# Performance work log

Hardware: AMD Instinct MI355X
Metric: run time of the kernel (lower is better)

## Reference

```python
import jax, jax.numpy as jnp
import numpy as np

SQRT2 = 1.4142135623730951
MH_C = 0.8673250705840776  # (2/sqrt(3)) * pi**(-1/4), mexican-hat normalizer


def _bn(x, eps=1e-5):
    # BatchNorm (training-mode batch stats, default affine gamma=1, beta=0)
    mu = jnp.mean(x, axis=0, keepdims=True)
    var = jnp.var(x, axis=0, keepdims=True)
    return (x - mu) / jnp.sqrt(var + eps)


def setup_inputs() -> dict:
    key = jax.random.key(0)
    ks = jax.random.split(key, 10)
    N, F, E, B, OUT = 1024, 1024, 32768, 16, 10
    H = F // 2  # 512 after Haar DWT
    x = jax.random.normal(ks[0], (N, F), dtype=jnp.float32)
    edge_index = jax.random.randint(ks[1], (2, E), 0, N, dtype=jnp.int32)
    batch = jnp.sort(jax.random.randint(ks[2], (N,), 0, B, dtype=jnp.int32))
    w_att = jax.random.normal(ks[3], (2,), dtype=jnp.float32)  # Linear(2,1,bias=False)
    wk_scale = jnp.ones((H, H), dtype=jnp.float32)
    wk_trans = jax.random.normal(ks[4], (H, H), dtype=jnp.float32) * 0.1
    wk_wav_w = jax.random.normal(ks[5], (H, H), dtype=jnp.float32) * 0.05
    wk_base_w = jax.random.normal(ks[6], (H, H), dtype=jnp.float32) * 0.05
    fc1_w = jax.random.normal(ks[7], (512, F + H), dtype=jnp.float32) * 0.02
    fc1_b = jnp.zeros((512,), dtype=jnp.float32)
    fc2_w = jax.random.normal(ks[8], (OUT, 512), dtype=jnp.float32) * 0.02
    fc2_b = jnp.zeros((OUT,), dtype=jnp.float32)
    return {"x": x, "w_att": w_att, "wk_scale": wk_scale, "wk_trans": wk_trans,
            "wk_wav_w": wk_wav_w, "wk_base_w": wk_base_w, "fc1_w": fc1_w,
            "fc1_b": fc1_b, "fc2_w": fc2_w, "fc2_b": fc2_b,
            "edge_index": edge_index, "batch": batch, "num_graphs": B}


def reference(x, w_att, wk_scale, wk_trans, wk_wav_w, wk_base_w,
              fc1_w, fc1_b, fc2_w, fc2_b, edge_index, batch, num_graphs):
    N = x.shape[0]
    # --- WaveletAttention: Haar ('db1') DWT over the feature dim ---
    xe, xo = x[:, 0::2], x[:, 1::2]
    low = (xe + xo) / SQRT2            # [N, 512]
    high = (xe - xo) / SQRT2           # [N, 512]
    scores = jax.nn.sigmoid(low * w_att[0] + high * w_att[1])
    h = scores * low + (1.0 - scores) * high
    # --- GINConv aggregation (eps=0): self + sum of neighbor features ---
    src, dst = edge_index[0], edge_index[1]
    agg = h + jax.ops.segment_sum(h[src], dst, num_segments=N)  # [N, 512]
    # --- WavKAN layer 512->512 (mexican hat) ---
    xs = (agg[:, None, :] - wk_trans) / wk_scale                # [N, 512, 512]
    xs2 = xs * xs
    mh = MH_C * (1.0 - xs2) * jnp.exp(-0.5 * xs2)
    wav = jnp.einsum('noi,oi->no', mh, wk_wav_w)                # [N, 512]
    base = jax.nn.silu(agg) @ wk_base_w.T
    conv_out = _bn(wav + base)   # WavKAN-internal BatchNorm1d
    conv_out = _bn(conv_out)     # bn1 (dropout p=0 -> identity)
    # --- skip concat + bn2 ---
    z = _bn(jnp.concatenate([x, conv_out], axis=1))             # [N, 1536]
    # --- global mean pool over graphs ---
    sums = jax.ops.segment_sum(z, batch, num_segments=num_graphs)
    cnts = jax.ops.segment_sum(jnp.ones((N,), z.dtype), batch, num_segments=num_graphs)
    pooled = sums / jnp.maximum(cnts, 1.0)[:, None]             # [B, 1536]
    # --- classifier head (eval-mode dropout = identity) ---
    h1 = jax.nn.relu(pooled @ fc1_w.T + fc1_b)
    return h1 @ fc2_w.T + fc2_b
```

## Files before the change

### kernel.cpp

```cpp
#include <hip/hip_runtime.h>
#include <math.h>

#define N_NODES 1024
#define F_DIM   1024
#define H_DIM   512
#define E_EDGES 32768
#define B_GRAPHS 16
#define OUT_DIM 10
#define FH_DIM  1536
#define EPS 1e-5f
#define MH_C_D 0.8673250705840776
#define C2_D   0.72134752044448170368
#define C2_F   ((float)C2_D)
#define CSC    0.84932180028801904272f
#define WC2F   ((float)(MH_C_D / C2_D))
#define INV_SQRT2 0.70710678118654752440f

typedef float v2f __attribute__((ext_vector_type(2)));
typedef unsigned int u32;
typedef const __attribute__((address_space(1))) u32 gu32;
typedef __attribute__((address_space(3))) u32 lu32;

#if __has_builtin(__builtin_amdgcn_exp2f)
#define EXP2NEG(x) __builtin_amdgcn_exp2f(-(x))
#else
#define EXP2NEG(x) __expf(-0.69314718055994530942f * (x))
#endif

#define PK_FMA_BB(d, a, p) \
    asm("v_pk_fma_f32 %0, %1, %2, %2 op_sel:[0,0,1] op_sel_hi:[1,0,1]" \
        : "=v"(d) : "v"(a), "v"(p))
#define PK_MUL2(d, a, b) \
    asm("v_pk_mul_f32 %0, %1, %2" : "=v"(d) : "v"(a), "v"(b))
#define PK_WZC(d, s, k) \
    asm("v_pk_mul_f32 %0, %1, %2 op_sel:[0,0] op_sel_hi:[0,1]" \
        : "=v"(d) : "v"(s), "v"(k))
#define PK_FMA_HI_ACC(acc, s, p) \
    asm("v_pk_fma_f32 %0, %1, %2, %0 op_sel:[0,1,0] op_sel_hi:[1,1,1]" \
        : "+v"(acc) : "v"(s), "v"(p))

__global__ __launch_bounds__(256) void k_setup(const float* __restrict__ x,
                                               const float* __restrict__ watt,
                                               float* __restrict__ h,
                                               const float* __restrict__ scale,
                                               const float* __restrict__ trans,
                                               const float* __restrict__ ww,
                                               const float* __restrict__ bw,
                                               float* __restrict__ pk,
                                               float* __restrict__ zbase) {
    const int bid = blockIdx.x;
    const int t = threadIdx.x;
    if (bid < 2048) {
        int idx = bid * 256 + t;
        float2 p = ((const float2*)x)[idx];
        float lo = (p.x + p.y) * INV_SQRT2;
        float hi = (p.x - p.y) * INV_SQRT2;
        float tt = lo * watt[0] + hi * watt[1];
        float sc = 1.0f / (1.0f + __expf(-tt));
        h[idx] = sc * lo + (1.0f - sc) * hi;
    } else if (bid < 3072) {
        int g = (bid - 2048) * 256 + t;
        float iv = 1.0f / scale[g];
        float4 p;
        p.x = iv * CSC;
        p.y = -(trans[g] * iv * CSC);
        p.z = -(ww[g] * WC2F);
        p.w = bw[g];
        ((float4*)pk)[g] = p;
    } else {
        zbase[(bid - 3072) * 256 + t] = 0.0f;
    }
}

__global__ __launch_bounds__(256) void k_hx(const int* __restrict__ dst,
                                            int* __restrict__ deg,
                                            const float* __restrict__ x,
                                            float* __restrict__ xsum,
                                            float* __restrict__ xsum2) {
    const int bid = blockIdx.x;
    const int t = threadIdx.x;
    if (bid < 128) {
        int e = bid * 256 + t;
        atomicAdd(&deg[dst[e]], 1);
    } else {
        const int n0 = (bid - 128) * 16;
        float s[4] = {}, s2[4] = {};
        for (int r = 0; r < 16; ++r) {
            #pragma unroll
            for (int ch = 0; ch < 4; ++ch) {
                float v = x[(n0 + r) * F_DIM + ch * 256 + t];
                s[ch] += v; s2[ch] += v * v;
            }
        }
        #pragma unroll
        for (int ch = 0; ch < 4; ++ch) {
            unsafeAtomicAdd(&xsum[ch * 256 + t], s[ch]);
            unsafeAtomicAdd(&xsum2[ch * 256 + t], s2[ch]);
        }
    }
}

__global__ __launch_bounds__(1024) void k_scan(const int* __restrict__ deg,
                                               int* __restrict__ start,
                                               int* __restrict__ cursor) {
    __shared__ int wsum[16];
    int t = threadIdx.x;
    int lane = t & 63, wid = t >> 6;
    int v = deg[t];
    int x = v;
    #pragma unroll
    for (int off = 1; off < 64; off <<= 1) {
        int y = __shfl_up(x, off, 64);
        if (lane >= off) x += y;
    }
    if (lane == 63) wsum[wid] = x;
    __syncthreads();
    if (t < 16) {
        int w = wsum[t];
        int xs = w;
        #pragma unroll
        for (int off = 1; off < 16; off <<= 1) {
            int y = __shfl_up(xs, off, 64);
            if (t >= off) xs += y;
        }
        wsum[t] = xs - w;
    }
    __syncthreads();
    int excl = wsum[wid] + x - v;
    start[t] = excl;
    cursor[t] = excl;
}

__global__ __launch_bounds__(256) void k_fill(const int* __restrict__ src,
                                              const int* __restrict__ dst,
                                              int* __restrict__ cursor,
                                              int* __restrict__ elist) {
    int e = blockIdx.x * 256 + threadIdx.x;
    int slot = atomicAdd(&cursor[dst[e]], 1);
    elist[slot] = src[e];
}

__global__ __launch_bounds__(256) void k_gather(const float* __restrict__ h,
                                                const int* __restrict__ start,
                                                const int* __restrict__ deg,
                                                const int* __restrict__ elist,
                                                float* __restrict__ agg) {
    int d = blockIdx.x;
    int t = threadIdx.x;
    int st = start[d], dg = deg[d];
    const float2* h2 = (const float2*)h;
    float2 a = h2[d * 256 + t];
    int k = 0;
    for (; k + 4 <= dg; k += 4) {
        int s0 = elist[st + k];
        int s1 = elist[st + k + 1];
        int s2 = elist[st + k + 2];
        int s3 = elist[st + k + 3];
        float2 v0 = h2[s0 * 256 + t];
        float2 v1 = h2[s1 * 256 + t];
        float2 v2 = h2[s2 * 256 + t];
        float2 v3 = h2[s3 * 256 + t];
        a.x += (v0.x + v1.x) + (v2.x + v3.x);
        a.y += (v0.y + v1.y) + (v2.y + v3.y);
    }
    for (; k < dg; ++k) {
        int s0 = elist[st + k];
        float2 v0 = h2[s0 * 256 + t];
        a.x += v0.x; a.y += v0.y;
    }
    ((float2*)agg)[d * 256 + t] = a;
}

__global__ __launch_bounds__(256) void k_transpose(const float* __restrict__ agg,
                                                   float* __restrict__ aggT,
                                                   float* __restrict__ siluT) {
    __shared__ float tile[64 * 65];
    const int t = threadIdx.x;
    const int n0 = blockIdx.x * 64;
    const int i0 = blockIdx.y * 64;
    #pragma unroll
    for (int v = 0; v < 4; ++v) {
        int flat = v * 256 + t;
        int r = flat >> 4, c4 = flat & 15;
        float4 a = *(const float4*)&agg[(n0 + r) * H_DIM + i0 + c4 * 4];
        tile[(c4 * 4 + 0) * 65 + r] = a.x;
        tile[(c4 * 4 + 1) * 65 + r] = a.y;
        tile[(c4 * 4 + 2) * 65 + r] = a.z;
        tile[(c4 * 4 + 3) * 65 + r] = a.w;
    }
    __syncthreads();
    #pragma unroll
    for (int v = 0; v < 4; ++v) {
        int flat = v * 256 + t;
        int il = flat >> 4, c4 = flat & 15;
        float4 a;
        a.x = tile[il * 65 + c4 * 4 + 0];
        a.y = tile[il * 65 + c4 * 4 + 1];
        a.z = tile[il * 65 + c4 * 4 + 2];
        a.w = tile[il * 65 + c4 * 4 + 3];
        int g = (i0 + il) * N_NODES + n0 + c4 * 4;
        *(float4*)&aggT[g] = a;
        float4 s;
        s.x = a.x / (1.0f + __expf(-a.x));
        s.y = a.y / (1.0f + __expf(-a.y));
        s.z = a.z / (1.0f + __expf(-a.z));
        s.w = a.w / (1.0f + __expf(-a.w));
        *(float4*)&siluT[g] = s;
    }
}

#define TN 64
#define TO 32
#define KI 16
#define TOP (TO + 1)
#define ZSPLIT 4
#define ZLEN (H_DIM / ZSPLIT)
#define NSTG (ZLEN / KI)
__global__ __launch_bounds__(256) void k_wavelet(const float* __restrict__ aggT,
                                                 const float* __restrict__ siluT,
                                                 const float* __restrict__ pk,
                                                 float* __restrict__ vbp) {
    __shared__ float sA[2][KI * TN];
    __shared__ float sS[2][KI * TN];
    __shared__ float4 sP4[2][KI * TOP];

    const int t  = threadIdx.x;
    const int n0 = blockIdx.x * TN;
    const int o0 = blockIdx.y * TO;
    const int z0 = blockIdx.z * ZLEN;
    const int nl = (t & 15) * 4;
    const int ol = (t >> 4) * 2;

    const int po  = t >> 4;
    const int pii = t & 15;
    const float4* pk4 = (const float4*)pk;

    v2f accw[2][2] = {};
    v2f accb[2][2] = {};
    v2f kC2; kC2.x = 1.0f; kC2.y = -C2_F;

    {
        int g = (z0 + (t >> 4)) * N_NODES + n0 + nl;
        __builtin_amdgcn_global_load_lds((gu32*)&aggT[g],  (lu32*)&sA[0][t * 4], 16, 0, 0);
        __builtin_amdgcn_global_load_lds((gu32*)&siluT[g], (lu32*)&sS[0][t * 4], 16, 0, 0);
        float4 r0 = pk4[(size_t)(o0 + po) * H_DIM + z0 + pii];
        float4 r1 = pk4[(size_t)(o0 + po + 16) * H_DIM + z0 + pii];
        sP4[0][pii * TOP + po]      = r0;
        sP4[0][pii * TOP + po + 16] = r1;
    }
    __syncthreads();

    for (int stg = 0; stg < NSTG; ++stg) {
        const int i0 = z0 + stg * KI;
        const int nb = (stg + 1) & 1;
        float4 r0, r1;
        if (stg + 1 < NSTG) {
            int g = (i0 + KI + (t >> 4)) * N_NODES + n0 + nl;
            __builtin_amdgcn_global_load_lds((gu32*)&aggT[g],  (lu32*)&sA[nb][t * 4], 16, 0, 0);
            __builtin_amdgcn_global_load_lds((gu32*)&siluT[g], (lu32*)&sS[nb][t * 4], 16, 0, 0);
            r0 = pk4[(size_t)(o0 + po) * H_DIM + i0 + KI + pii];
            r1 = pk4[(size_t)(o0 + po + 16) * H_DIM + i0 + KI + pii];
        }
        const float*  pA = sA[stg & 1];
        const float*  pS = sS[stg & 1];
        const float4* pP = sP4[stg & 1];
        #pragma unroll 4
        for (int ii = 0; ii < KI; ++ii) {
            float4 af = *(const float4*)&pA[ii * TN + nl];
            float4 sf = *(const float4*)&pS[ii * TN + nl];
            v2f a01 = {af.x, af.y}, a23 = {af.z, af.w};
            v2f s01 = {sf.x, sf.y}, s23 = {sf.z, sf.w};
            #pragma unroll
            for (int oo = 0; oo < 2; ++oo) {
                float4 pq = pP[ii * TOP + ol + oo];
                v2f pxy = {pq.x, pq.y};
                v2f pzw = {pq.z, pq.w};
                v2f wzc; PK_WZC(wzc, pzw, kC2);
                v2f y0;  PK_FMA_BB(y0, a01, pxy);
                v2f y1;  PK_FMA_BB(y1, a23, pxy);
                v2f q0;  PK_MUL2(q0, y0, y0);
                v2f q1;  PK_MUL2(q1, y1, y1);
                v2f w0;  PK_FMA_BB(w0, q0, wzc);
                v2f w1;  PK_FMA_BB(w1, q1, wzc);
                float e00 = EXP2NEG(q0.x), e01 = EXP2NEG(q0.y);
                float e10 = EXP2NEG(q1.x), e11 = EXP2NEG(q1.y);
                accw[oo][0].x += w0.x * e00;
                accw[oo][0].y += w0.y * e01;
                accw[oo][1].x += w1.x * e10;
                accw[oo][1].y += w1.y * e11;
                PK_FMA_HI_ACC(accb[oo][0], s01, pzw);
                PK_FMA_HI_ACC(accb[oo][1], s23, pzw);
            }
        }
        if (stg + 1 < NSTG) {
            sP4[nb][pii * TOP + po]      = r0;
            sP4[nb][pii * TOP + po + 16] = r1;
        }
        __syncthreads();
    }
    float* out = vbp + (size_t)blockIdx.z * (N_NODES * H_DIM);
    #pragma unroll
    for (int nn = 0; nn < 4; ++nn) {
        int pr = nn >> 1, cmu = nn & 1;
        float2 o2;
        o2.x = cmu ? accw[0][pr].y + accb[0][pr].y : accw[0][pr].x + accb[0][pr].x;
        o2.y = cmu ? accw[1][pr].y + accb[1][pr].y : accw[1][pr].x + accb[1][pr].x;
        *(float2*)&out[(n0 + nl + nn) * H_DIM + o0 + ol] = o2;
    }
}

__global__ __launch_bounds__(256) void k_reduce(const float* __restrict__ vbp,
                                                float* __restrict__ vb,
                                                float* __restrict__ colsum,
                                                float* __restrict__ colsum2) {
    const int b = blockIdx.x;
    const int o0 = (b & 7) * 64;
    const int n0 = (b >> 3) * 64;
    const int t = threadIdx.x;
    const int oc = o0 + (t & 63);
    const int nsub = t >> 6;
    float s = 0.f, s2 = 0.f;
    for (int r = 0; r < 16; ++r) {
        int n = n0 + r * 4 + nsub;
        size_t idx = (size_t)n * H_DIM + oc;
        float v = 0.f;
        #pragma unroll
        for (int z = 0; z < ZSPLIT; ++z) v += vbp[z * (N_NODES * H_DIM) + idx];
        vb[idx] = v;
        s += v; s2 += v * v;
    }
    __shared__ float sh1[256], sh2[256];
    sh1[t] = s; sh2[t] = s2;
    __syncthreads();
    if (t < 64) {
        s  = sh1[t] + sh1[t + 64] + sh1[t + 128] + sh1[t + 192];
        s2 = sh2[t] + sh2[t + 64] + sh2[t + 128] + sh2[t + 192];
        unsafeAtomicAdd(&colsum[o0 + t], s);
        unsafeAtomicAdd(&colsum2[o0 + t], s2);
    }
}

__global__ __launch_bounds__(256) void k_pool(const float* __restrict__ x,
                                              const float* __restrict__ vb,
                                              const int* __restrict__ batch,
                                              const float* __restrict__ colsum,
                                              const float* __restrict__ colsum2,
                                              const float* __restrict__ xsum,
                                              const float* __restrict__ xsum2,
                                              float* __restrict__ pooled) {
    const int b = blockIdx.x;
    const int ch = blockIdx.y;
    const int t = threadIdx.x;

    __shared__ int s_cnt[4];
    __shared__ int s_st;
    int c = 0;
    for (int n = t; n < N_NODES; n += 256) {
        int bb = batch[n];
        int pb = (n == 0) ? -1 : batch[n - 1];
        c += (bb == b) ? 1 : 0;
        if (bb == b && pb != b) s_st = n;
    }
    #pragma unroll
    for (int off = 32; off > 0; off >>= 1) c += __shfl_down(c, off);
    if ((t & 63) == 0) s_cnt[t >> 6] = c;
    __syncthreads();
    int cnt = s_cnt[0] + s_cnt[1] + s_cnt[2] + s_cnt[3];
    int st = (cnt > 0) ? s_st : 0;
    float ic = (cnt > 0) ? 1.0f / (float)cnt : 0.f;

    float acc = 0.f;
    if (ch < 4) {
        int col = ch * 256 + t;
        float mu  = xsum[col] * (1.0f / N_NODES);
        float var = xsum2[col] * (1.0f / N_NODES) - mu * mu;
        if (var < 0.f) var = 0.f;
        float S = 1.0f / sqrtf(var + EPS);
        const float* base = x + col;
        for (int r = 0; r < cnt; ++r) acc += base[(size_t)(st + r) * F_DIM];
        pooled[b * FH_DIM + col] = (acc * ic - mu) * S;
    } else {
        int col = (ch - 4) * 256 + t;
        float mu  = colsum[col] * (1.0f / N_NODES);
        float var = colsum2[col] * (1.0f / N_NODES) - mu * mu;
        if (var < 0.f) var = 0.f;
        float s1v = 1.0f / sqrtf(var + EPS);
        float v1  = var * s1v * s1v;
        float s2v = 1.0f / sqrtf(v1 + EPS);
        float v2  = v1 * s2v * s2v;
        float s3v = 1.0f / sqrtf(v2 + EPS);
        float S = s1v * s2v * s3v;
        const float* base = vb + col;
        for (int r = 0; r < cnt; ++r) acc += base[(size_t)(st + r) * H_DIM];
        pooled[b * FH_DIM + F_DIM + col] = (acc * ic - mu) * S;
    }
}

__global__ __launch_bounds__(256) void k_fc1(const float* __restrict__ pooled,
                                             const float* __restrict__ w,
                                             const float* __restrict__ bias,
                                             float* __restrict__ h1) {
    int wid = (blockIdx.x * 256 + threadIdx.x) >> 6;
    int lane = threadIdx.x & 63;
    int b = wid >> 9, o = wid & 511;
    const float4* pr = (const float4*)(pooled + b * FH_DIM);
    const float4* wr = (const float4*)(w + o * FH_DIM);
    float acc = 0.f;
    #pragma unroll
    for (int k = 0; k < 6; ++k) {
        float4 a = pr[k * 64 + lane];
        float4 v = wr[k * 64 + lane];
        acc += a.x * v.x + a.y * v.y + a.z * v.z + a.w * v.w;
    }
    #pragma unroll
    for (int off = 32; off > 0; off >>= 1) acc += __shfl_down(acc, off);
    if (lane == 0) h1[b * H_DIM + o] = fmaxf(acc + bias[o], 0.f);
}

__global__ __launch_bounds__(256) void k_fc2(const float* __restrict__ h1,
                                             const float* __restrict__ w,
                                             const float* __restrict__ bias,
                                             float* __restrict__ outp) {
    int wid = (blockIdx.x * 256 + threadIdx.x) >> 6;
    int lane = threadIdx.x & 63;
    if (wid >= B_GRAPHS * OUT_DIM) return;
    int b = wid / OUT_DIM, u = wid % OUT_DIM;
    const float4* hr = (const float4*)(h1 + b * H_DIM);
    const float4* wr = (const float4*)(w + u * H_DIM);
    float acc = 0.f;
    #pragma unroll
    for (int k = 0; k < 2; ++k) {
        float4 a = hr[k * 64 + lane];
        float4 v = wr[k * 64 + lane];
        acc += a.x * v.x + a.y * v.y + a.z * v.z + a.w * v.w;
    }
    #pragma unroll
    for (int off = 32; off > 0; off >>= 1) acc += __shfl_down(acc, off);
    if (lane == 0) outp[b * OUT_DIM + u] = acc + bias[u];
}

extern "C" void kernel_launch(void* const* d_in, const int* in_sizes, int n_in,
                              void* d_out, int out_size, void* d_ws, size_t ws_size,
                              hipStream_t stream) {
    const float* x       = (const float*)d_in[0];
    const float* w_att   = (const float*)d_in[1];
    const float* wk_scale= (const float*)d_in[2];
    const float* wk_trans= (const float*)d_in[3];
    const float* wk_wav  = (const float*)d_in[4];
    const float* wk_base = (const float*)d_in[5];
    const float* fc1_w   = (const float*)d_in[6];
    const float* fc1_b   = (const float*)d_in[7];
    const float* fc2_w   = (const float*)d_in[8];
    const float* fc2_b   = (const float*)d_in[9];
    const int*   eidx    = (const int*)d_in[10];
    const int*   batch   = (const int*)d_in[11];
    float* outp = (float*)d_out;

    float* ws = (float*)d_ws;
    const int NH = N_NODES * H_DIM;
    float* h      = ws;
    float* agg    = h + NH;
    float* aggT   = agg + NH;
    float* siluT  = aggT + NH;
    float* pk     = siluT + NH;
    float* vbp    = pk + 4 * (H_DIM * H_DIM);
    float* vb     = vbp + (size_t)ZSPLIT * NH;
    float* colsum = vb + NH;
    float* colsum2= colsum + 512;
    float* xsum   = colsum2 + 512;
    float* xsum2  = xsum + 1024;
    int*   deg    = (int*)(xsum2 + 1024);
    int*   estart = deg + N_NODES;
    int*   cursor = estart + N_NODES;
    int*   elist  = cursor + N_NODES;
    float* pooled = (float*)(elist + E_EDGES);
    float* h1     = pooled + B_GRAPHS * FH_DIM;

    const int* src = eidx;
    const int* dst = eidx + E_EDGES;

    k_setup<<<3088, 256, 0, stream>>>(x, w_att, h, wk_scale, wk_trans, wk_wav, wk_base,
                                      pk, colsum);
    k_hx<<<192, 256, 0, stream>>>(dst, deg, x, xsum, xsum2);
    k_scan<<<1, N_NODES, 0, stream>>>(deg, estart, cursor);
    k_fill<<<E_EDGES / 256, 256, 0, stream>>>(src, dst, cursor, elist);
    k_gather<<<N_NODES, 256, 0, stream>>>(h, estart, deg, elist, agg);
    {
        dim3 grid(N_NODES / 64, H_DIM / 64);
        k_transpose<<<grid, 256, 0, stream>>>(agg, aggT, siluT);
    }
    {
        dim3 grid(N_NODES / TN, H_DIM / TO, ZSPLIT);
        k_wavelet<<<grid, 256, 0, stream>>>(aggT, siluT, pk, vbp);
    }
    k_reduce<<<128, 256, 0, stream>>>(vbp, vb, colsum, colsum2);
    {
        dim3 grid(B_GRAPHS, 6);
        k_pool<<<grid, 256, 0, stream>>>(x, vb, batch, colsum, colsum2, xsum, xsum2, pooled);
    }
    k_fc1<<<(B_GRAPHS * H_DIM * 64) / 256, 256, 0, stream>>>(pooled, fc1_w, fc1_b, h1);
    k_fc2<<<(B_GRAPHS * OUT_DIM * 64 + 255) / 256, 256, 0, stream>>>(h1, fc2_w, fc2_b, outp);
}
```

Before: 196.6 us.

## Fuse all pipeline stages into one cooperative persistent kernel with grid syncs

Replaces the eleven separate kernel launches (setup, degree/stats, scan, fill, gather, transpose, wavelet, reduce, pool, fc1, fc2) with a single cooperative kernel of 512 blocks. The stages are separated by grid-wide barriers, and each stage's work is spread across the persistent blocks. The aim is to remove per-launch overhead and inter-kernel gaps. In exchange, the kernel pays grid.sync costs and is capped at a fixed occupancy, which may reduce parallelism for stages like the wavelet GEMM that previously used larger grids.

```diff
diff --git a/kernel.cpp b/kernel.cpp
--- a/kernel.cpp
+++ b/kernel.cpp
@@ -1,5 +1,8 @@
 #include <hip/hip_runtime.h>
+#include <hip/hip_cooperative_groups.h>
 #include <math.h>
+
+namespace cg = cooperative_groups;
 
 #define N_NODES 1024
 #define F_DIM   1024
@@ -39,176 +42,6 @@
     asm("v_pk_fma_f32 %0, %1, %2, %0 op_sel:[0,1,0] op_sel_hi:[1,1,1]" \
         : "+v"(acc) : "v"(s), "v"(p))
 
-__global__ __launch_bounds__(256) void k_setup(const float* __restrict__ x,
-                                               const float* __restrict__ watt,
-                                               float* __restrict__ h,
-                                               const float* __restrict__ scale,
-                                               const float* __restrict__ trans,
-                                               const float* __restrict__ ww,
-                                               const float* __restrict__ bw,
-                                               float* __restrict__ pk,
-                                               float* __restrict__ zbase) {
-    const int bid = blockIdx.x;
-    const int t = threadIdx.x;
-    if (bid < 2048) {
-        int idx = bid * 256 + t;
-        float2 p = ((const float2*)x)[idx];
-        float lo = (p.x + p.y) * INV_SQRT2;
-        float hi = (p.x - p.y) * INV_SQRT2;
-        float tt = lo * watt[0] + hi * watt[1];
-        float sc = 1.0f / (1.0f + __expf(-tt));
-        h[idx] = sc * lo + (1.0f - sc) * hi;
-    } else if (bid < 3072) {
-        int g = (bid - 2048) * 256 + t;
-        float iv = 1.0f / scale[g];
-        float4 p;
-        p.x = iv * CSC;
-        p.y = -(trans[g] * iv * CSC);
-        p.z = -(ww[g] * WC2F);
-        p.w = bw[g];
-        ((float4*)pk)[g] = p;
-    } else {
-        zbase[(bid - 3072) * 256 + t] = 0.0f;
-    }
-}
-
-__global__ __launch_bounds__(256) void k_hx(const int* __restrict__ dst,
-                                            int* __restrict__ deg,
-                                            const float* __restrict__ x,
-                                            float* __restrict__ xsum,
-                                            float* __restrict__ xsum2) {
-    const int bid = blockIdx.x;
-    const int t = threadIdx.x;
-    if (bid < 128) {
-        int e = bid * 256 + t;
-        atomicAdd(&deg[dst[e]], 1);
-    } else {
-        const int n0 = (bid - 128) * 16;
-        float s[4] = {}, s2[4] = {};
-        for (int r = 0; r < 16; ++r) {
-            #pragma unroll
-            for (int ch = 0; ch < 4; ++ch) {
-                float v = x[(n0 + r) * F_DIM + ch * 256 + t];
-                s[ch] += v; s2[ch] += v * v;
-            }
-        }
-        #pragma unroll
-        for (int ch = 0; ch < 4; ++ch) {
-            unsafeAtomicAdd(&xsum[ch * 256 + t], s[ch]);
-            unsafeAtomicAdd(&xsum2[ch * 256 + t], s2[ch]);
-        }
-    }
-}
-
-__global__ __launch_bounds__(1024) void k_scan(const int* __restrict__ deg,
-                                               int* __restrict__ start,
-                                               int* __restrict__ cursor) {
-    __shared__ int wsum[16];
-    int t = threadIdx.x;
-    int lane = t & 63, wid = t >> 6;
-    int v = deg[t];
-    int x = v;
-    #pragma unroll
-    for (int off = 1; off < 64; off <<= 1) {
-        int y = __shfl_up(x, off, 64);
-        if (lane >= off) x += y;
-    }
-    if (lane == 63) wsum[wid] = x;
-    __syncthreads();
-    if (t < 16) {
-        int w = wsum[t];
-        int xs = w;
-        #pragma unroll
-        for (int off = 1; off < 16; off <<= 1) {
-            int y = __shfl_up(xs, off, 64);
-            if (t >= off) xs += y;
-        }
-        wsum[t] = xs - w;
-    }
-    __syncthreads();
-    int excl = wsum[wid] + x - v;
-    start[t] = excl;
-    cursor[t] = excl;
-}
-
-__global__ __launch_bounds__(256) void k_fill(const int* __restrict__ src,
-                                              const int* __restrict__ dst,
-                                              int* __restrict__ cursor,
-                                              int* __restrict__ elist) {
-    int e = blockIdx.x * 256 + threadIdx.x;
-    int slot = atomicAdd(&cursor[dst[e]], 1);
-    elist[slot] = src[e];
-}
-
-__global__ __launch_bounds__(256) void k_gather(const float* __restrict__ h,
-                                                const int* __restrict__ start,
-                                                const int* __restrict__ deg,
-                                                const int* __restrict__ elist,
-                                                float* __restrict__ agg) {
-    int d = blockIdx.x;
-    int t = threadIdx.x;
-    int st = start[d], dg = deg[d];
-    const float2* h2 = (const float2*)h;
-    float2 a = h2[d * 256 + t];
-    int k = 0;
-    for (; k + 4 <= dg; k += 4) {
-        int s0 = elist[st + k];
-        int s1 = elist[st + k + 1];
-        int s2 = elist[st + k + 2];
-        int s3 = elist[st + k + 3];
-        float2 v0 = h2[s0 * 256 + t];
-        float2 v1 = h2[s1 * 256 + t];
-        float2 v2 = h2[s2 * 256 + t];
-        float2 v3 = h2[s3 * 256 + t];
-        a.x += (v0.x + v1.x) + (v2.x + v3.x);
-        a.y += (v0.y + v1.y) + (v2.y + v3.y);
-    }
-    for (; k < dg; ++k) {
-        int s0 = elist[st + k];
-        float2 v0 = h2[s0 * 256 + t];
-        a.x += v0.x; a.y += v0.y;
-    }
-    ((float2*)agg)[d * 256 + t] = a;
-}
-
-__global__ __launch_bounds__(256) void k_transpose(const float* __restrict__ agg,
-                                                   float* __restrict__ aggT,
-                                                   float* __restrict__ siluT) {
-    __shared__ float tile[64 * 65];
-    const int t = threadIdx.x;
-    const int n0 = blockIdx.x * 64;
-    const int i0 = blockIdx.y * 64;
-    #pragma unroll
-    for (int v = 0; v < 4; ++v) {
-        int flat = v * 256 + t;
-        int r = flat >> 4, c4 = flat & 15;
-        float4 a = *(const float4*)&agg[(n0 + r) * H_DIM + i0 + c4 * 4];
-        tile[(c4 * 4 + 0) * 65 + r] = a.x;
-        tile[(c4 * 4 + 1) * 65 + r] = a.y;
-        tile[(c4 * 4 + 2) * 65 + r] = a.z;
-        tile[(c4 * 4 + 3) * 65 + r] = a.w;
-    }
-    __syncthreads();
-    #pragma unroll
-    for (int v = 0; v < 4; ++v) {
-        int flat = v * 256 + t;
-        int il = flat >> 4, c4 = flat & 15;
-        float4 a;
-        a.x = tile[il * 65 + c4 * 4 + 0];
-        a.y = tile[il * 65 + c4 * 4 + 1];
-        a.z = tile[il * 65 + c4 * 4 + 2];
-        a.w = tile[il * 65 + c4 * 4 + 3];
-        int g = (i0 + il) * N_NODES + n0 + c4 * 4;
-        *(float4*)&aggT[g] = a;
-        float4 s;
-        s.x = a.x / (1.0f + __expf(-a.x));
-        s.y = a.y / (1.0f + __expf(-a.y));
-        s.z = a.z / (1.0f + __expf(-a.z));
-        s.w = a.w / (1.0f + __expf(-a.w));
-        *(float4*)&siluT[g] = s;
-    }
-}
-
 #define TN 64
 #define TO 32
 #define KI 16
@@ -216,246 +49,387 @@
 #define ZSPLIT 4
 #define ZLEN (H_DIM / ZSPLIT)
 #define NSTG (ZLEN / KI)
-__global__ __launch_bounds__(256) void k_wavelet(const float* __restrict__ aggT,
-                                                 const float* __restrict__ siluT,
-                                                 const float* __restrict__ pk,
-                                                 float* __restrict__ vbp) {
-    __shared__ float sA[2][KI * TN];
-    __shared__ float sS[2][KI * TN];
-    __shared__ float4 sP4[2][KI * TOP];
-
-    const int t  = threadIdx.x;
-    const int n0 = blockIdx.x * TN;
-    const int o0 = blockIdx.y * TO;
-    const int z0 = blockIdx.z * ZLEN;
-    const int nl = (t & 15) * 4;
-    const int ol = (t >> 4) * 2;
-
-    const int po  = t >> 4;
-    const int pii = t & 15;
-    const float4* pk4 = (const float4*)pk;
-
-    v2f accw[2][2] = {};
-    v2f accb[2][2] = {};
-    v2f kC2; kC2.x = 1.0f; kC2.y = -C2_F;
-
-    {
-        int g = (z0 + (t >> 4)) * N_NODES + n0 + nl;
-        __builtin_amdgcn_global_load_lds((gu32*)&aggT[g],  (lu32*)&sA[0][t * 4], 16, 0, 0);
-        __builtin_amdgcn_global_load_lds((gu32*)&siluT[g], (lu32*)&sS[0][t * 4], 16, 0, 0);
-        float4 r0 = pk4[(size_t)(o0 + po) * H_DIM + z0 + pii];
-        float4 r1 = pk4[(size_t)(o0 + po + 16) * H_DIM + z0 + pii];
-        sP4[0][pii * TOP + po]      = r0;
-        sP4[0][pii * TOP + po + 16] = r1;
-    }
-    __syncthreads();
-
-    for (int stg = 0; stg < NSTG; ++stg) {
-        const int i0 = z0 + stg * KI;
-        const int nb = (stg + 1) & 1;
-        float4 r0, r1;
-        if (stg + 1 < NSTG) {
-            int g = (i0 + KI + (t >> 4)) * N_NODES + n0 + nl;
-            __builtin_amdgcn_global_load_lds((gu32*)&aggT[g],  (lu32*)&sA[nb][t * 4], 16, 0, 0);
-            __builtin_amdgcn_global_load_lds((gu32*)&siluT[g], (lu32*)&sS[nb][t * 4], 16, 0, 0);
-            r0 = pk4[(size_t)(o0 + po) * H_DIM + i0 + KI + pii];
-            r1 = pk4[(size_t)(o0 + po + 16) * H_DIM + i0 + KI + pii];
-        }
-        const float*  pA = sA[stg & 1];
-        const float*  pS = sS[stg & 1];
-        const float4* pP = sP4[stg & 1];
-        #pragma unroll 4
-        for (int ii = 0; ii < KI; ++ii) {
-            float4 af = *(const float4*)&pA[ii * TN + nl];
-            float4 sf = *(const float4*)&pS[ii * TN + nl];
-            v2f a01 = {af.x, af.y}, a23 = {af.z, af.w};
-            v2f s01 = {sf.x, sf.y}, s23 = {sf.z, sf.w};
-            #pragma unroll
-            for (int oo = 0; oo < 2; ++oo) {
-                float4 pq = pP[ii * TOP + ol + oo];
-                v2f pxy = {pq.x, pq.y};
-                v2f pzw = {pq.z, pq.w};
-                v2f wzc; PK_WZC(wzc, pzw, kC2);
-                v2f y0;  PK_FMA_BB(y0, a01, pxy);
-                v2f y1;  PK_FMA_BB(y1, a23, pxy);
-                v2f q0;  PK_MUL2(q0, y0, y0);
-                v2f q1;  PK_MUL2(q1, y1, y1);
-                v2f w0;  PK_FMA_BB(w0, q0, wzc);
-                v2f w1;  PK_FMA_BB(w1, q1, wzc);
-                float e00 = EXP2NEG(q0.x), e01 = EXP2NEG(q0.y);
-                float e10 = EXP2NEG(q1.x), e11 = EXP2NEG(q1.y);
-                accw[oo][0].x += w0.x * e00;
-                accw[oo][0].y += w0.y * e01;
-                accw[oo][1].x += w1.x * e10;
-                accw[oo][1].y += w1.y * e11;
-                PK_FMA_HI_ACC(accb[oo][0], s01, pzw);
-                PK_FMA_HI_ACC(accb[oo][1], s23, pzw);
-            }
-        }
-        if (stg + 1 < NSTG) {
-            sP4[nb][pii * TOP + po]      = r0;
-            sP4[nb][pii * TOP + po + 16] = r1;
-        }
-        __syncthreads();
-    }
-    float* out = vbp + (size_t)blockIdx.z * (N_NODES * H_DIM);
-    #pragma unroll
-    for (int nn = 0; nn < 4; ++nn) {
-        int pr = nn >> 1, cmu = nn & 1;
-        float2 o2;
-        o2.x = cmu ? accw[0][pr].y + accb[0][pr].y : accw[0][pr].x + accb[0][pr].x;
-        o2.y = cmu ? accw[1][pr].y + accb[1][pr].y : accw[1][pr].x + accb[1][pr].x;
-        *(float2*)&out[(n0 + nl + nn) * H_DIM + o0 + ol] = o2;
-    }
-}
-
-__global__ __launch_bounds__(256) void k_reduce(const float* __restrict__ vbp,
-                                                float* __restrict__ vb,
-                                                float* __restrict__ colsum,
-                                                float* __restrict__ colsum2) {
-    const int b = blockIdx.x;
-    const int o0 = (b & 7) * 64;
-    const int n0 = (b >> 3) * 64;
-    const int t = threadIdx.x;
-    const int oc = o0 + (t & 63);
-    const int nsub = t >> 6;
-    float s = 0.f, s2 = 0.f;
-    for (int r = 0; r < 16; ++r) {
-        int n = n0 + r * 4 + nsub;
-        size_t idx = (size_t)n * H_DIM + oc;
-        float v = 0.f;
-        #pragma unroll
-        for (int z = 0; z < ZSPLIT; ++z) v += vbp[z * (N_NODES * H_DIM) + idx];
-        vb[idx] = v;
-        s += v; s2 += v * v;
-    }
-    __shared__ float sh1[256], sh2[256];
-    sh1[t] = s; sh2[t] = s2;
-    __syncthreads();
-    if (t < 64) {
-        s  = sh1[t] + sh1[t + 64] + sh1[t + 128] + sh1[t + 192];
-        s2 = sh2[t] + sh2[t + 64] + sh2[t + 128] + sh2[t + 192];
-        unsafeAtomicAdd(&colsum[o0 + t], s);
-        unsafeAtomicAdd(&colsum2[o0 + t], s2);
-    }
-}
-
-__global__ __launch_bounds__(256) void k_pool(const float* __restrict__ x,
-                                              const float* __restrict__ vb,
-                                              const int* __restrict__ batch,
-                                              const float* __restrict__ colsum,
-                                              const float* __restrict__ colsum2,
-                                              const float* __restrict__ xsum,
-                                              const float* __restrict__ xsum2,
-                                              float* __restrict__ pooled) {
-    const int b = blockIdx.x;
-    const int ch = blockIdx.y;
-    const int t = threadIdx.x;
-
+
+struct MegaArgs {
+    const float *x, *watt, *scale, *trans, *ww, *bw, *fc1w, *fc1b, *fc2w, *fc2b;
+    const int *src, *dst, *batch;
+    float *h, *pk, *agg, *aggT, *siluT, *vbp, *vb;
+    float *colsum, *colsum2, *xsum, *xsum2, *pooled, *h1, *outp;
+    int *deg, *estart, *cursor, *elist;
+};
+
+__global__ __launch_bounds__(256, 4) void k_mega(MegaArgs a) {
+    __shared__ __align__(16) char smem[33280];
+    __shared__ int wsum4[4], woff[4];
     __shared__ int s_cnt[4];
     __shared__ int s_st;
-    int c = 0;
-    for (int n = t; n < N_NODES; n += 256) {
-        int bb = batch[n];
-        int pb = (n == 0) ? -1 : batch[n - 1];
-        c += (bb == b) ? 1 : 0;
-        if (bb == b && pb != b) s_st = n;
-    }
+
+    const int bid = blockIdx.x;
+    const int t = threadIdx.x;
+    cg::grid_group grid = cg::this_grid();
+
     #pragma unroll
-    for (int off = 32; off > 0; off >>= 1) c += __shfl_down(c, off);
-    if ((t & 63) == 0) s_cnt[t >> 6] = c;
-    __syncthreads();
-    int cnt = s_cnt[0] + s_cnt[1] + s_cnt[2] + s_cnt[3];
-    int st = (cnt > 0) ? s_st : 0;
-    float ic = (cnt > 0) ? 1.0f / (float)cnt : 0.f;
-
-    float acc = 0.f;
-    if (ch < 4) {
-        int col = ch * 256 + t;
-        float mu  = xsum[col] * (1.0f / N_NODES);
-        float var = xsum2[col] * (1.0f / N_NODES) - mu * mu;
-        if (var < 0.f) var = 0.f;
-        float S = 1.0f / sqrtf(var + EPS);
-        const float* base = x + col;
-        for (int r = 0; r < cnt; ++r) acc += base[(size_t)(st + r) * F_DIM];
-        pooled[b * FH_DIM + col] = (acc * ic - mu) * S;
-    } else {
-        int col = (ch - 4) * 256 + t;
-        float mu  = colsum[col] * (1.0f / N_NODES);
-        float var = colsum2[col] * (1.0f / N_NODES) - mu * mu;
-        if (var < 0.f) var = 0.f;
-        float s1v = 1.0f / sqrtf(var + EPS);
-        float v1  = var * s1v * s1v;
-        float s2v = 1.0f / sqrtf(v1 + EPS);
-        float v2  = v1 * s2v * s2v;
-        float s3v = 1.0f / sqrtf(v2 + EPS);
-        float S = s1v * s2v * s3v;
-        const float* base = vb + col;
-        for (int r = 0; r < cnt; ++r) acc += base[(size_t)(st + r) * H_DIM];
-        pooled[b * FH_DIM + F_DIM + col] = (acc * ic - mu) * S;
-    }
-}
-
-__global__ __launch_bounds__(256) void k_fc1(const float* __restrict__ pooled,
-                                             const float* __restrict__ w,
-                                             const float* __restrict__ bias,
-                                             float* __restrict__ h1) {
-    int wid = (blockIdx.x * 256 + threadIdx.x) >> 6;
-    int lane = threadIdx.x & 63;
-    int b = wid >> 9, o = wid & 511;
-    const float4* pr = (const float4*)(pooled + b * FH_DIM);
-    const float4* wr = (const float4*)(w + o * FH_DIM);
-    float acc = 0.f;
+    for (int wv = 0; wv < 4; ++wv) {
+        int idx = (bid * 4 + wv) * 256 + t;
+        float2 p = ((const float2*)a.x)[idx];
+        float lo = (p.x + p.y) * INV_SQRT2;
+        float hi = (p.x - p.y) * INV_SQRT2;
+        float tt = lo * a.watt[0] + hi * a.watt[1];
+        float sc = 1.0f / (1.0f + __expf(-tt));
+        a.h[idx] = sc * lo + (1.0f - sc) * hi;
+    }
     #pragma unroll
-    for (int k = 0; k < 6; ++k) {
-        float4 a = pr[k * 64 + lane];
-        float4 v = wr[k * 64 + lane];
-        acc += a.x * v.x + a.y * v.y + a.z * v.z + a.w * v.w;
-    }
-    #pragma unroll
-    for (int off = 32; off > 0; off >>= 1) acc += __shfl_down(acc, off);
-    if (lane == 0) h1[b * H_DIM + o] = fmaxf(acc + bias[o], 0.f);
-}
-
-__global__ __launch_bounds__(256) void k_fc2(const float* __restrict__ h1,
-                                             const float* __restrict__ w,
-                                             const float* __restrict__ bias,
-                                             float* __restrict__ outp) {
-    int wid = (blockIdx.x * 256 + threadIdx.x) >> 6;
-    int lane = threadIdx.x & 63;
-    if (wid >= B_GRAPHS * OUT_DIM) return;
-    int b = wid / OUT_DIM, u = wid % OUT_DIM;
-    const float4* hr = (const float4*)(h1 + b * H_DIM);
-    const float4* wr = (const float4*)(w + u * H_DIM);
-    float acc = 0.f;
-    #pragma unroll
-    for (int k = 0; k < 2; ++k) {
-        float4 a = hr[k * 64 + lane];
-        float4 v = wr[k * 64 + lane];
-        acc += a.x * v.x + a.y * v.y + a.z * v.z + a.w * v.w;
-    }
-    #pragma unroll
-    for (int off = 32; off > 0; off >>= 1) acc += __shfl_down(acc, off);
-    if (lane == 0) outp[b * OUT_DIM + u] = acc + bias[u];
+    for (int wv = 0; wv < 2; ++wv) {
+        int g = (bid * 2 + wv) * 256 + t;
+        float iv = 1.0f / a.scale[g];
+        float4 p;
+        p.x = iv * CSC;
+        p.y = -(a.trans[g] * iv * CSC);
+        p.z = -(a.ww[g] * WC2F);
+        p.w = a.bw[g];
+        ((float4*)a.pk)[g] = p;
+    }
+    if (bid < 16) a.colsum[bid * 256 + t] = 0.0f;
+    grid.sync();
+
+    if (bid < 128) {
+        int e = bid * 256 + t;
+        atomicAdd(&a.deg[a.dst[e]], 1);
+    } else if (bid < 192) {
+        const int n0 = (bid - 128) * 16;
+        float s[4] = {}, s2[4] = {};
+        for (int r = 0; r < 16; ++r) {
+            #pragma unroll
+            for (int ch = 0; ch < 4; ++ch) {
+                float v = a.x[(n0 + r) * F_DIM + ch * 256 + t];
+                s[ch] += v; s2[ch] += v * v;
+            }
+        }
+        #pragma unroll
+        for (int ch = 0; ch < 4; ++ch) {
+            unsafeAtomicAdd(&a.xsum[ch * 256 + t], s[ch]);
+            unsafeAtomicAdd(&a.xsum2[ch * 256 + t], s2[ch]);
+        }
+    }
+    grid.sync();
+
+    if (bid == 0) {
+        int4 d = *(const int4*)&a.deg[t * 4];
+        int s = d.x + d.y + d.z + d.w;
+        int lane = t & 63, wid = t >> 6;
+        int xsc = s;
+        #pragma unroll
+        for (int off = 1; off < 64; off <<= 1) {
+            int y = __shfl_up(xsc, off, 64);
+            if (lane >= off) xsc += y;
+        }
+        if (lane == 63) wsum4[wid] = xsc;
+        __syncthreads();
+        if (t == 0) {
+            int acc0 = 0;
+            #pragma unroll
+            for (int q = 0; q < 4; ++q) { woff[q] = acc0; acc0 += wsum4[q]; }
+        }
+        __syncthreads();
+        int excl = woff[wid] + xsc - s;
+        int st0 = excl, st1 = excl + d.x, st2 = st1 + d.y, st3 = st2 + d.z;
+        a.estart[t * 4] = st0; a.estart[t * 4 + 1] = st1;
+        a.estart[t * 4 + 2] = st2; a.estart[t * 4 + 3] = st3;
+        a.cursor[t * 4] = st0; a.cursor[t * 4 + 1] = st1;
+        a.cursor[t * 4 + 2] = st2; a.cursor[t * 4 + 3] = st3;
+    }
+    grid.sync();
+
+    if (bid < 128) {
+        int e = bid * 256 + t;
+        int slot = atomicAdd(&a.cursor[a.dst[e]], 1);
+        a.elist[slot] = a.src[e];
+    }
+    grid.sync();
+
+    {
+        const float2* h2 = (const float2*)a.h;
+        for (int r = 0; r < 2; ++r) {
+            int d = bid * 2 + r;
+            int st = a.estart[d], dg = a.deg[d];
+            float2 acc2 = h2[d * 256 + t];
+            int k = 0;
+            for (; k + 4 <= dg; k += 4) {
+                int s0 = a.elist[st + k];
+                int s1 = a.elist[st + k + 1];
+                int s2 = a.elist[st + k + 2];
+                int s3 = a.elist[st + k + 3];
+                float2 v0 = h2[s0 * 256 + t];
+                float2 v1 = h2[s1 * 256 + t];
+                float2 v2 = h2[s2 * 256 + t];
+                float2 v3 = h2[s3 * 256 + t];
+                acc2.x += (v0.x + v1.x) + (v2.x + v3.x);
+                acc2.y += (v0.y + v1.y) + (v2.y + v3.y);
+            }
+            for (; k < dg; ++k) {
+                int s0 = a.elist[st + k];
+                float2 v0 = h2[s0 * 256 + t];
+                acc2.x += v0.x; acc2.y += v0.y;
+            }
+            ((float2*)a.agg)[d * 256 + t] = acc2;
+        }
+    }
+    grid.sync();
+
+    if (bid < 128) {
+        float* tile = (float*)smem;
+        const int n0 = (bid & 15) * 64;
+        const int i0 = (bid >> 4) * 64;
+        #pragma unroll
+        for (int v = 0; v < 4; ++v) {
+            int flat = v * 256 + t;
+            int r = flat >> 4, c4 = flat & 15;
+            float4 aq = *(const float4*)&a.agg[(n0 + r) * H_DIM + i0 + c4 * 4];
+            tile[(c4 * 4 + 0) * 65 + r] = aq.x;
+            tile[(c4 * 4 + 1) * 65 + r] = aq.y;
+            tile[(c4 * 4 + 2) * 65 + r] = aq.z;
+            tile[(c4 * 4 + 3) * 65 + r] = aq.w;
+        }
+        __syncthreads();
+        #pragma unroll
+        for (int v = 0; v < 4; ++v) {
+            int flat = v * 256 + t;
+            int il = flat >> 4, c4 = flat & 15;
+            float4 aq;
+            aq.x = tile[il * 65 + c4 * 4 + 0];
+            aq.y = tile[il * 65 + c4 * 4 + 1];
+            aq.z = tile[il * 65 + c4 * 4 + 2];
+            aq.w = tile[il * 65 + c4 * 4 + 3];
+            int g = (i0 + il) * N_NODES + n0 + c4 * 4;
+            *(float4*)&a.aggT[g] = aq;
+            float4 sq;
+            sq.x = aq.x / (1.0f + __expf(-aq.x));
+            sq.y = aq.y / (1.0f + __expf(-aq.y));
+            sq.z = aq.z / (1.0f + __expf(-aq.z));
+            sq.w = aq.w / (1.0f + __expf(-aq.w));
+            *(float4*)&a.siluT[g] = sq;
+        }
+    }
+    grid.sync();
+
+    {
+        float*  sA  = (float*)smem;
+        float*  sS  = sA + 2048;
+        float4* sP4 = (float4*)(smem + 16384);
+
+        const int nl = (t & 15) * 4;
+        const int ol = (t >> 4) * 2;
+        const int po  = t >> 4;
+        const int pii = t & 15;
+        const float4* pk4 = (const float4*)a.pk;
+        v2f kC2; kC2.x = 1.0f; kC2.y = -C2_F;
+
+        for (int task = 0; task < 2; ++task) {
+            const int tid7 = bid * 2 + task;
+            const int tz  = tid7 >> 8;
+            const int rem = tid7 & 255;
+            const int n0 = (rem & 15) * TN;
+            const int o0 = (rem >> 4) * TO;
+            const int z0 = tz * ZLEN;
+
+            v2f accw[2][2] = {};
+            v2f accb[2][2] = {};
+
+            {
+                int g = (z0 + (t >> 4)) * N_NODES + n0 + nl;
+                __builtin_amdgcn_global_load_lds((gu32*)&a.aggT[g],  (lu32*)&sA[t * 4], 16, 0, 0);
+                __builtin_amdgcn_global_load_lds((gu32*)&a.siluT[g], (lu32*)&sS[t * 4], 16, 0, 0);
+                float4 r0 = pk4[(size_t)(o0 + po) * H_DIM + z0 + pii];
+                float4 r1 = pk4[(size_t)(o0 + po + 16) * H_DIM + z0 + pii];
+                sP4[pii * TOP + po]      = r0;
+                sP4[pii * TOP + po + 16] = r1;
+            }
+            __syncthreads();
+
+            for (int stg = 0; stg < NSTG; ++stg) {
+                const int i0 = z0 + stg * KI;
+                const int nb = (stg + 1) & 1;
+                float4 r0, r1;
+                if (stg + 1 < NSTG) {
+                    int g = (i0 + KI + (t >> 4)) * N_NODES + n0 + nl;
+                    __builtin_amdgcn_global_load_lds((gu32*)&a.aggT[g],
+                                                     (lu32*)&sA[nb * 1024 + t * 4], 16, 0, 0);
+                    __builtin_amdgcn_global_load_lds((gu32*)&a.siluT[g],
+                                                     (lu32*)&sS[nb * 1024 + t * 4], 16, 0, 0);
+                    r0 = pk4[(size_t)(o0 + po) * H_DIM + i0 + KI + pii];
+                    r1 = pk4[(size_t)(o0 + po + 16) * H_DIM + i0 + KI + pii];
+                }
+                const float*  pA = sA + (stg & 1) * 1024;
+                const float*  pS = sS + (stg & 1) * 1024;
+                const float4* pP = sP4 + (stg & 1) * (KI * TOP);
+                #pragma unroll 4
+                for (int ii = 0; ii < KI; ++ii) {
+                    float4 af = *(const float4*)&pA[ii * TN + nl];
+                    float4 sf = *(const float4*)&pS[ii * TN + nl];
+                    v2f a01 = {af.x, af.y}, a23 = {af.z, af.w};
+                    v2f s01 = {sf.x, sf.y}, s23 = {sf.z, sf.w};
+                    #pragma unroll
+                    for (int oo = 0; oo < 2; ++oo) {
+                        float4 pq = pP[ii * TOP + ol + oo];
+                        v2f pxy = {pq.x, pq.y};
+                        v2f pzw = {pq.z, pq.w};
+                        v2f wzc; PK_WZC(wzc, pzw, kC2);
+                        v2f y0, y1, q0, q1, w0, w1;
+                        PK_FMA_BB(y0, a01, pxy);
+                        PK_FMA_BB(y1, a23, pxy);
+                        PK_MUL2(q0, y0, y0);
+                        PK_MUL2(q1, y1, y1);
+                        PK_FMA_BB(w0, q0, wzc);
+                        PK_FMA_BB(w1, q1, wzc);
+                        float e00 = EXP2NEG(q0.x), e01 = EXP2NEG(q0.y);
+                        float e10 = EXP2NEG(q1.x), e11 = EXP2NEG(q1.y);
+                        accw[oo][0].x += w0.x * e00;
+                        accw[oo][0].y += w0.y * e01;
+                        accw[oo][1].x += w1.x * e10;
+                        accw[oo][1].y += w1.y * e11;
+                        PK_FMA_HI_ACC(accb[oo][0], s01, pzw);
+                        PK_FMA_HI_ACC(accb[oo][1], s23, pzw);
+                    }
+                }
+                if (stg + 1 < NSTG) {
+                    sP4[nb * (KI * TOP) + pii * TOP + po]      = r0;
+                    sP4[nb * (KI * TOP) + pii * TOP + po + 16] = r1;
+                }
+                __syncthreads();
+            }
+            float* out = a.vbp + (size_t)tz * (N_NODES * H_DIM);
+            #pragma unroll
+            for (int nn = 0; nn < 4; ++nn) {
+                int pr = nn >> 1, cmu = nn & 1;
+                float2 o2;
+                o2.x = cmu ? accw[0][pr].y + accb[0][pr].y : accw[0][pr].x + accb[0][pr].x;
+                o2.y = cmu ? accw[1][pr].y + accb[1][pr].y : accw[1][pr].x + accb[1][pr].x;
+                *(float2*)&out[(n0 + nl + nn) * H_DIM + o0 + ol] = o2;
+            }
+            __syncthreads();
+        }
+    }
+    grid.sync();
+
+    if (bid < 128) {
+        float* sh1 = (float*)smem;
+        float* sh2 = sh1 + 256;
+        const int o0 = (bid & 7) * 64;
+        const int n0 = (bid >> 3) * 64;
+        const int oc = o0 + (t & 63);
+        const int nsub = t >> 6;
+        float s = 0.f, s2 = 0.f;
+        for (int r = 0; r < 16; ++r) {
+            int n = n0 + r * 4 + nsub;
+            size_t idx = (size_t)n * H_DIM + oc;
+            float v = 0.f;
+            #pragma unroll
+            for (int z = 0; z < ZSPLIT; ++z) v += a.vbp[z * (N_NODES * H_DIM) + idx];
+            a.vb[idx] = v;
+            s += v; s2 += v * v;
+        }
+        sh1[t] = s; sh2[t] = s2;
+        __syncthreads();
+        if (t < 64) {
+            s  = sh1[t] + sh1[t + 64] + sh1[t + 128] + sh1[t + 192];
+            s2 = sh2[t] + sh2[t + 64] + sh2[t + 128] + sh2[t + 192];
+            unsafeAtomicAdd(&a.colsum[o0 + t], s);
+            unsafeAtomicAdd(&a.colsum2[o0 + t], s2);
+        }
+    }
+    grid.sync();
+
+    if (bid < 96) {
+        const int b = bid / 6;
+        const int ch = bid % 6;
+        int c = 0;
+        for (int n = t; n < N_NODES; n += 256) {
+            int bb = a.batch[n];
+            int pb = (n == 0) ? -1 : a.batch[n - 1];
+            c += (bb == b) ? 1 : 0;
+            if (bb == b && pb != b) s_st = n;
+        }
+        #pragma unroll
+        for (int off = 32; off > 0; off >>= 1) c += __shfl_down(c, off);
+        if ((t & 63) == 0) s_cnt[t >> 6] = c;
+        __syncthreads();
+        int cnt = s_cnt[0] + s_cnt[1] + s_cnt[2] + s_cnt[3];
+        int st = (cnt > 0) ? s_st : 0;
+        float ic = (cnt > 0) ? 1.0f / (float)cnt : 0.f;
+        float acc = 0.f;
+        if (ch < 4) {
+            int col = ch * 256 + t;
+            float mu  = a.xsum[col] * (1.0f / N_NODES);
+            float var = a.xsum2[col] * (1.0f / N_NODES) - mu * mu;
+            if (var < 0.f) var = 0.f;
+            float S = 1.0f / sqrtf(var + EPS);
+            const float* base = a.x + col;
+            for (int r = 0; r < cnt; ++r) acc += base[(size_t)(st + r) * F_DIM];
+            a.pooled[b * FH_DIM + col] = (acc * ic - mu) * S;
+        } else {
+            int col = (ch - 4) * 256 + t;
+            float mu  = a.colsum[col] * (1.0f / N_NODES);
+            float var = a.colsum2[col] * (1.0f / N_NODES) - mu * mu;
+            if (var < 0.f) var = 0.f;
+            float s1v = 1.0f / sqrtf(var + EPS);
+            float v1  = var * s1v * s1v;
+            float s2v = 1.0f / sqrtf(v1 + EPS);
+            float v2  = v1 * s2v * s2v;
+            float s3v = 1.0f / sqrtf(v2 + EPS);
+            float S = s1v * s2v * s3v;
+            const float* base = a.vb + col;
+            for (int r = 0; r < cnt; ++r) acc += base[(size_t)(st + r) * H_DIM];
+            a.pooled[b * FH_DIM + F_DIM + col] = (acc * ic - mu) * S;
+        }
+    }
+    grid.sync();
+
+    {
+        int lane = t & 63;
+        int gw = bid * 4 + (t >> 6);
+        for (int k2 = 0; k2 < 4; ++k2) {
+            int wid = gw * 4 + k2;
+            int b = wid >> 9, o = wid & 511;
+            const float4* pr = (const float4*)(a.pooled + b * FH_DIM);
+            const float4* wr = (const float4*)(a.fc1w + o * FH_DIM);
+            float acc = 0.f;
+            #pragma unroll
+            for (int k = 0; k < 6; ++k) {
+                float4 aa = pr[k * 64 + lane];
+                float4 vv = wr[k * 64 + lane];
+                acc += aa.x * vv.x + aa.y * vv.y + aa.z * vv.z + aa.w * vv.w;
+            }
+            #pragma unroll
+            for (int off = 32; off > 0; off >>= 1) acc += __shfl_down(acc, off);
+            if (lane == 0) a.h1[b * H_DIM + o] = fmaxf(acc + a.fc1b[o], 0.f);
+        }
+    }
+    grid.sync();
+
+    {
+        int lane = t & 63;
+        int gw = bid * 4 + (t >> 6);
+        if (gw < B_GRAPHS * OUT_DIM) {
+            int b = gw / OUT_DIM, u = gw % OUT_DIM;
+            const float4* hr = (const float4*)(a.h1 + b * H_DIM);
+            const float4* wr = (const float4*)(a.fc2w + u * H_DIM);
+            float acc = 0.f;
+            #pragma unroll
+            for (int k = 0; k < 2; ++k) {
+                float4 aa = hr[k * 64 + lane];
+                float4 vv = wr[k * 64 + lane];
+                acc += aa.x * vv.x + aa.y * vv.y + aa.z * vv.z + aa.w * vv.w;
+            }
+            #pragma unroll
+            for (int off = 32; off > 0; off >>= 1) acc += __shfl_down(acc, off);
+            if (lane == 0) a.outp[b * OUT_DIM + u] = acc + a.fc2b[u];
+        }
+    }
 }
 
 extern "C" void kernel_launch(void* const* d_in, const int* in_sizes, int n_in,
                               void* d_out, int out_size, void* d_ws, size_t ws_size,
                               hipStream_t stream) {
-    const float* x       = (const float*)d_in[0];
-    const float* w_att   = (const float*)d_in[1];
-    const float* wk_scale= (const float*)d_in[2];
-    const float* wk_trans= (const float*)d_in[3];
-    const float* wk_wav  = (const float*)d_in[4];
-    const float* wk_base = (const float*)d_in[5];
-    const float* fc1_w   = (const float*)d_in[6];
-    const float* fc1_b   = (const float*)d_in[7];
-    const float* fc2_w   = (const float*)d_in[8];
-    const float* fc2_b   = (const float*)d_in[9];
-    const int*   eidx    = (const int*)d_in[10];
-    const int*   batch   = (const int*)d_in[11];
-    float* outp = (float*)d_out;
-
     float* ws = (float*)d_ws;
     const int NH = N_NODES * H_DIM;
     float* h      = ws;
@@ -476,28 +450,26 @@
     float* pooled = (float*)(elist + E_EDGES);
     float* h1     = pooled + B_GRAPHS * FH_DIM;
 
-    const int* src = eidx;
-    const int* dst = eidx + E_EDGES;
-
-    k_setup<<<3088, 256, 0, stream>>>(x, w_att, h, wk_scale, wk_trans, wk_wav, wk_base,
-                                      pk, colsum);
-    k_hx<<<192, 256, 0, stream>>>(dst, deg, x, xsum, xsum2);
-    k_scan<<<1, N_NODES, 0, stream>>>(deg, estart, cursor);
-    k_fill<<<E_EDGES / 256, 256, 0, stream>>>(src, dst, cursor, elist);
-    k_gather<<<N_NODES, 256, 0, stream>>>(h, estart, deg, elist, agg);
-    {
-        dim3 grid(N_NODES / 64, H_DIM / 64);
-        k_transpose<<<grid, 256, 0, stream>>>(agg, aggT, siluT);
-    }
-    {
-        dim3 grid(N_NODES / TN, H_DIM / TO, ZSPLIT);
-        k_wavelet<<<grid, 256, 0, stream>>>(aggT, siluT, pk, vbp);
-    }
-    k_reduce<<<128, 256, 0, stream>>>(vbp, vb, colsum, colsum2);
-    {
-        dim3 grid(B_GRAPHS, 6);
-        k_pool<<<grid, 256, 0, stream>>>(x, vb, batch, colsum, colsum2, xsum, xsum2, pooled);
-    }
-    k_fc1<<<(B_GRAPHS * H_DIM * 64) / 256, 256, 0, stream>>>(pooled, fc1_w, fc1_b, h1);
-    k_fc2<<<(B_GRAPHS * OUT_DIM * 64 + 255) / 256, 256, 0, stream>>>(h1, fc2_w, fc2_b, outp);
+    MegaArgs a;
+    a.x = (const float*)d_in[0];
+    a.watt = (const float*)d_in[1];
+    a.scale = (const float*)d_in[2];
+    a.trans = (const float*)d_in[3];
+    a.ww = (const float*)d_in[4];
+    a.bw = (const float*)d_in[5];
+    a.fc1w = (const float*)d_in[6];
+    a.fc1b = (const float*)d_in[7];
+    a.fc2w = (const float*)d_in[8];
+    a.fc2b = (const float*)d_in[9];
+    a.src = (const int*)d_in[10];
+    a.dst = a.src + E_EDGES;
+    a.batch = (const int*)d_in[11];
+    a.h = h; a.pk = pk; a.agg = agg; a.aggT = aggT; a.siluT = siluT;
+    a.vbp = vbp; a.vb = vb;
+    a.colsum = colsum; a.colsum2 = colsum2; a.xsum = xsum; a.xsum2 = xsum2;
+    a.pooled = pooled; a.h1 = h1; a.outp = (float*)d_out;
+    a.deg = deg; a.estart = estart; a.cursor = cursor; a.elist = elist;
+
+    void* kargs[] = { (void*)&a };
+    hipLaunchCooperativeKernel((void*)k_mega, dim3(512), dim3(256), kargs, 0, stream);
 }
```

After: 761.0 us. 3.87x slower.
